# Optimization experiments

Measured on AMD Instinct MI355X. Metric: run time of the kernel, lower is better.

## Reference

```python
import jax, jax.numpy as jnp
import numpy as np

N = 50000
E = 640000
F_IN = 128
F_OUT = 128


def setup_inputs() -> dict:
    key = jax.random.key(0)
    k1, k2, k3, k4, k5 = jax.random.split(key, 5)
    x = jax.random.normal(k1, (N, F_IN), dtype=jnp.float32)
    edge_index = jax.random.randint(k2, (2, E), 0, N, dtype=jnp.int64)
    s = 1.0 / np.sqrt(F_IN)
    W_l = jax.random.uniform(k3, (F_IN, F_OUT), minval=-s, maxval=s, dtype=jnp.float32)
    W_r = jax.random.uniform(k4, (F_IN, F_OUT), minval=-s, maxval=s, dtype=jnp.float32)
    b = jax.random.uniform(k5, (F_OUT,), minval=-s, maxval=s, dtype=jnp.float32)
    return {"x": x, "edge_index": edge_index, "W_l": W_l, "W_r": W_r, "b": b}


def reference(x, edge_index, W_l, W_r, b):
    src, dst = edge_index[0], edge_index[1]
    # gather source-node features along edges: [E, F_in]
    msgs = x[src]
    # mean aggregation at destination nodes
    summed = jax.ops.segment_sum(msgs, dst, num_segments=N)          # [N, F_in]
    counts = jax.ops.segment_sum(jnp.ones((E,), jnp.float32), dst, num_segments=N)
    mean_nb = summed / jnp.maximum(counts, 1.0)[:, None]
    # SAGEConv: lin_l(aggregated) + lin_r(self), bias on lin_l only
    out = mean_nb @ W_l + x @ W_r + b
    return jax.nn.relu(out)
```

## Files before the change

kernel.cpp:

```cpp
#include <hip/hip_runtime.h>

#define N_NODES 50000
#define E_EDGES 640000
#define F 128

typedef __attribute__((ext_vector_type(8))) short short8;
typedef __attribute__((ext_vector_type(4))) float f32x4;

#define DEG_OFF 0
#define OFF_OFF 200704
#define CUR_OFF 401408
#define BSUM_OFF 601600
#define WF_OFF 603648
#define SRC_OFF 734720
#define XBF_OFF 3294720
#define MBF_OFF 16094720
#define WS_NEED_FULL 28894720ULL

#define XCAST_BLKS 3125
#define WPREP_BLKS 16
#define HIST_BLKS 2048
#define PREP_GRID (XCAST_BLKS + WPREP_BLKS + HIST_BLKS)

__device__ __forceinline__ unsigned short f2bf(float f) {
    unsigned int u = __builtin_bit_cast(unsigned int, f);
    u += 0x7FFFu + ((u >> 16) & 1u);
    return (unsigned short)(u >> 16);
}
__device__ __forceinline__ float bfhi2f(unsigned int hi16) {
    return __builtin_bit_cast(float, hi16 & 0xFFFF0000u);
}

__global__ __launch_bounds__(256) void gnn_prep(
    const float* __restrict__ x, const int* __restrict__ ei,
    const float* __restrict__ Wl, const float* __restrict__ Wr,
    short* __restrict__ Wf, unsigned short* __restrict__ xbf,
    int* __restrict__ deg, int full) {
    const int bid = blockIdx.x;
    const int t = threadIdx.x;
    if (bid < XCAST_BLKS) {
        if (!full) return;
        const size_t i = ((size_t)bid * 256 + t) * 8;
        const float4 a0 = *reinterpret_cast<const float4*>(x + i);
        const float4 a1 = *reinterpret_cast<const float4*>(x + i + 4);
        short8 v;
        v[0] = (short)f2bf(a0.x); v[1] = (short)f2bf(a0.y);
        v[2] = (short)f2bf(a0.z); v[3] = (short)f2bf(a0.w);
        v[4] = (short)f2bf(a1.x); v[5] = (short)f2bf(a1.y);
        v[6] = (short)f2bf(a1.z); v[7] = (short)f2bf(a1.w);
        *reinterpret_cast<short8*>((short*)xbf + i) = v;
    } else if (bid < XCAST_BLKS + WPREP_BLKS) {
        const int tid = (bid - XCAST_BLKS) * 256 + t;
        const int lane = tid & 63;
        const int frag = tid >> 6;
        const int kstep = frag >> 3;
        const int ct = frag & 7;
        const int kb = kstep * 32 + (lane >> 4) * 8;
        const int c = ct * 16 + (lane & 15);
        short8 v;
#pragma unroll
        for (int j = 0; j < 8; ++j) {
            const int k = kb + j;
            const float f = (k < F) ? Wl[k * F + c] : Wr[(k - F) * F + c];
            v[j] = (short)f2bf(f);
        }
        *reinterpret_cast<short8*>(Wf + (size_t)tid * 8) = v;
    } else {
        const int i = (bid - XCAST_BLKS - WPREP_BLKS) * 256 + t;
        const int stride = HIST_BLKS * 256;
        for (int e = i; e < E_EDGES; e += stride)
            atomicAdd(&deg[ei[E_EDGES + e]], 1);
    }
}

__global__ __launch_bounds__(256) void gnn_scan_a(const int* __restrict__ deg,
                                                  int* __restrict__ off,
                                                  int* __restrict__ bsum) {
    __shared__ int s[256];
    const int t = threadIdx.x;
    const int i = blockIdx.x * 256 + t;
    const int v = (i < N_NODES) ? deg[i] : 0;
    s[t] = v;
    __syncthreads();
    for (int d = 1; d < 256; d <<= 1) {
        const int u = (t >= d) ? s[t - d] : 0;
        __syncthreads();
        s[t] += u;
        __syncthreads();
    }
    if (i < N_NODES) off[i] = s[t] - v;
    if (t == 255) bsum[blockIdx.x] = s[255];
}

__global__ __launch_bounds__(256) void gnn_scan2(const int* __restrict__ bsum,
                                                 int* __restrict__ off,
                                                 int* __restrict__ cur) {
    __shared__ int s[256];
    const int t = threadIdx.x;
    const int bid = blockIdx.x;
    s[t] = (t < 196) ? bsum[t] : 0;
    __syncthreads();
    for (int d = 1; d < 256; d <<= 1) {
        const int u = (t >= d) ? s[t - d] : 0;
        __syncthreads();
        s[t] += u;
        __syncthreads();
    }
    const int myPre = (bid == 0) ? 0 : s[bid - 1];
    const int i = bid * 256 + t;
    if (i < N_NODES) {
        const int o = off[i] + myPre;
        off[i] = o;
        cur[i] = o;
    }
    if (bid == 0 && t == 0) off[N_NODES] = s[195];
}

__global__ __launch_bounds__(256) void gnn_fill(const int* __restrict__ ei,
                                                int* __restrict__ cur,
                                                int* __restrict__ srcs) {
    const int i = blockIdx.x * blockDim.x + threadIdx.x;
    const int stride = gridDim.x * blockDim.x;
    for (int e = i; e < E_EDGES; e += stride) {
        const int d = ei[E_EDGES + e];
        const int p = atomicAdd(&cur[d], 1);
        srcs[p] = ei[e];
    }
}

__global__ __launch_bounds__(256) void gnn_aggregate_bf(
    const unsigned short* __restrict__ xbf, const int* __restrict__ off,
    const int* __restrict__ srcs, unsigned short* __restrict__ mbf) {
    const int node = blockIdx.x * 4 + (threadIdx.x >> 6);
    if (node >= N_NODES) return;
    const int lane = threadIdx.x & 63;
    const int half = lane >> 5;
    const int l32 = lane & 31;
    const int o0 = off[node];
    const int o1 = off[node + 1];
    const unsigned short* xb = xbf + (size_t)l32 * 4;
    f32x4 acc0 = {0.f, 0.f, 0.f, 0.f}, acc1 = {0.f, 0.f, 0.f, 0.f};
    f32x4 acc2 = {0.f, 0.f, 0.f, 0.f}, acc3 = {0.f, 0.f, 0.f, 0.f};
    int j = o0;
    for (; j + 8 <= o1; j += 8) {
        const uint2 a = *reinterpret_cast<const uint2*>(xb + (size_t)srcs[j + half] * F);
        const uint2 b = *reinterpret_cast<const uint2*>(xb + (size_t)srcs[j + 2 + half] * F);
        const uint2 c = *reinterpret_cast<const uint2*>(xb + (size_t)srcs[j + 4 + half] * F);
        const uint2 d = *reinterpret_cast<const uint2*>(xb + (size_t)srcs[j + 6 + half] * F);
        acc0[0] += bfhi2f(a.x << 16); acc0[1] += bfhi2f(a.x);
        acc0[2] += bfhi2f(a.y << 16); acc0[3] += bfhi2f(a.y);
        acc1[0] += bfhi2f(b.x << 16); acc1[1] += bfhi2f(b.x);
        acc1[2] += bfhi2f(b.y << 16); acc1[3] += bfhi2f(b.y);
        acc2[0] += bfhi2f(c.x << 16); acc2[1] += bfhi2f(c.x);
        acc2[2] += bfhi2f(c.y << 16); acc2[3] += bfhi2f(c.y);
        acc3[0] += bfhi2f(d.x << 16); acc3[1] += bfhi2f(d.x);
        acc3[2] += bfhi2f(d.y << 16); acc3[3] += bfhi2f(d.y);
    }
    for (; j + 4 <= o1; j += 4) {
        const uint2 a = *reinterpret_cast<const uint2*>(xb + (size_t)srcs[j + half] * F);
        const uint2 b = *reinterpret_cast<const uint2*>(xb + (size_t)srcs[j + 2 + half] * F);
        acc0[0] += bfhi2f(a.x << 16); acc0[1] += bfhi2f(a.x);
        acc0[2] += bfhi2f(a.y << 16); acc0[3] += bfhi2f(a.y);
        acc1[0] += bfhi2f(b.x << 16); acc1[1] += bfhi2f(b.x);
        acc1[2] += bfhi2f(b.y << 16); acc1[3] += bfhi2f(b.y);
    }
    for (; j < o1; j += 2) {
        const int jj = j + half;
        const uint2 a = *reinterpret_cast<const uint2*>(
            xb + (size_t)srcs[(jj < o1) ? jj : o0] * F);
        if (jj < o1) {
            acc0[0] += bfhi2f(a.x << 16); acc0[1] += bfhi2f(a.x);
            acc0[2] += bfhi2f(a.y << 16); acc0[3] += bfhi2f(a.y);
        }
    }
    acc0 += acc1 + acc2 + acc3;
    f32x4 o;
    o[0] = __shfl_xor(acc0[0], 32, 64);
    o[1] = __shfl_xor(acc0[1], 32, 64);
    o[2] = __shfl_xor(acc0[2], 32, 64);
    o[3] = __shfl_xor(acc0[3], 32, 64);
    acc0 += o;
    if (half == 0) {
        const float inv = 1.0f / (float)max(o1 - o0, 1);
        acc0 *= inv;
        ushort4 m;
        m.x = f2bf(acc0[0]); m.y = f2bf(acc0[1]);
        m.z = f2bf(acc0[2]); m.w = f2bf(acc0[3]);
        *reinterpret_cast<ushort4*>(mbf + (size_t)node * F + l32 * 4) = m;
    }
}

__global__ __launch_bounds__(256) void gnn_finalize_bf(
    const unsigned short* __restrict__ xbf, const unsigned short* __restrict__ mbf,
    const short* __restrict__ Wf, const float* __restrict__ bias,
    float* __restrict__ out) {
    const int t = threadIdx.x;
    const int lane = t & 63;
    const int wv = t >> 6;
    const int r0 = blockIdx.x * 64 + wv * 16;
    const int rl = lane & 15;
    const int kg = lane >> 4;
    const int arow = r0 + rl;
    const int arow_c = (arow < N_NODES) ? arow : (N_NODES - 1);

    f32x4 acc[8];
#pragma unroll
    for (int ct = 0; ct < 8; ++ct) acc[ct] = (f32x4){0.f, 0.f, 0.f, 0.f};

#pragma unroll
    for (int kstep = 0; kstep < 8; ++kstep) {
        const int k0 = kstep * 32 + kg * 8;
        const unsigned short* asrc =
            (kstep < 4) ? (mbf + (size_t)arow_c * F + k0)
                        : (xbf + (size_t)arow_c * F + (k0 - F));
        const short8 af = *reinterpret_cast<const short8*>(asrc);
#pragma unroll
        for (int ct = 0; ct < 8; ++ct) {
            const short8 bf = *reinterpret_cast<const short8*>(
                Wf + (size_t)((kstep * 8 + ct) * 64 + lane) * 8);
            acc[ct] = __builtin_amdgcn_mfma_f32_16x16x32_bf16(af, bf, acc[ct],
                                                              0, 0, 0);
        }
    }

#pragma unroll
    for (int ct = 0; ct < 8; ++ct) {
        const int c = ct * 16 + rl;
        const float bv = bias[c];
#pragma unroll
        for (int r = 0; r < 4; ++r) {
            const int row = r0 + kg * 4 + r;
            if (row < N_NODES)
                out[(size_t)row * F + c] = fmaxf(acc[ct][r] + bv, 0.0f);
        }
    }
}

__global__ __launch_bounds__(256) void gnn_aggregate(
    const float* __restrict__ x, const int* __restrict__ off,
    const int* __restrict__ srcs, float* __restrict__ out) {
    const int node = blockIdx.x * 4 + (threadIdx.x >> 6);
    if (node >= N_NODES) return;
    const int lane = threadIdx.x & 63;
    const int half = lane >> 5;
    const int l32 = lane & 31;
    const int o0 = off[node];
    const int o1 = off[node + 1];
    f32x4 acc0 = {0.f, 0.f, 0.f, 0.f};
    f32x4 acc1 = {0.f, 0.f, 0.f, 0.f};
    int j = o0;
    for (; j + 4 <= o1; j += 4) {
        const int sA = srcs[j + half];
        const int sB = srcs[j + 2 + half];
        acc0 += *reinterpret_cast<const f32x4*>(x + (size_t)sA * F + l32 * 4);
        acc1 += *reinterpret_cast<const f32x4*>(x + (size_t)sB * F + l32 * 4);
    }
    for (; j < o1; j += 2) {
        const int jj = j + half;
        const int s = srcs[(jj < o1) ? jj : o0];
        f32x4 v = *reinterpret_cast<const f32x4*>(x + (size_t)s * F + l32 * 4);
        if (jj >= o1) v = (f32x4){0.f, 0.f, 0.f, 0.f};
        acc0 += v;
    }
    acc0 += acc1;
    f32x4 o;
    o[0] = __shfl_xor(acc0[0], 32, 64);
    o[1] = __shfl_xor(acc0[1], 32, 64);
    o[2] = __shfl_xor(acc0[2], 32, 64);
    o[3] = __shfl_xor(acc0[3], 32, 64);
    acc0 += o;
    if (half == 0) {
        const float inv = 1.0f / (float)max(o1 - o0, 1);
        acc0 *= inv;
        *reinterpret_cast<f32x4*>(out + (size_t)node * F + l32 * 4) = acc0;
    }
}

__global__ __launch_bounds__(256) void gnn_finalize_mfma(
    const float* __restrict__ x, const short* __restrict__ Wf,
    const float* __restrict__ bias, float* __restrict__ out) {
    const int t = threadIdx.x;
    const int lane = t & 63;
    const int wv = t >> 6;
    const int r0 = blockIdx.x * 64 + wv * 16;
    const int rl = lane & 15;
    const int kg = lane >> 4;
    const int arow = r0 + rl;
    const int arow_c = (arow < N_NODES) ? arow : (N_NODES - 1);
    f32x4 acc[8];
#pragma unroll
    for (int ct = 0; ct < 8; ++ct) acc[ct] = (f32x4){0.f, 0.f, 0.f, 0.f};
#pragma unroll
    for (int kstep = 0; kstep < 8; ++kstep) {
        const int k0 = kstep * 32 + kg * 8;
        const float* asrc = (kstep < 4) ? (out + (size_t)arow_c * F + k0)
                                        : (x + (size_t)arow_c * F + (k0 - F));
        const float4 a0 = *reinterpret_cast<const float4*>(asrc);
        const float4 a1 = *reinterpret_cast<const float4*>(asrc + 4);
        short8 af;
        af[0] = (short)f2bf(a0.x); af[1] = (short)f2bf(a0.y);
        af[2] = (short)f2bf(a0.z); af[3] = (short)f2bf(a0.w);
        af[4] = (short)f2bf(a1.x); af[5] = (short)f2bf(a1.y);
        af[6] = (short)f2bf(a1.z); af[7] = (short)f2bf(a1.w);
#pragma unroll
        for (int ct = 0; ct < 8; ++ct) {
            const short8 bf = *reinterpret_cast<const short8*>(
                Wf + (size_t)((kstep * 8 + ct) * 64 + lane) * 8);
            acc[ct] = __builtin_amdgcn_mfma_f32_16x16x32_bf16(af, bf, acc[ct],
                                                              0, 0, 0);
        }
    }
#pragma unroll
    for (int ct = 0; ct < 8; ++ct) {
        const int c = ct * 16 + rl;
        const float bv = bias[c];
#pragma unroll
        for (int r = 0; r < 4; ++r) {
            const int row = r0 + kg * 4 + r;
            if (row < N_NODES)
                out[(size_t)row * F + c] = fmaxf(acc[ct][r] + bv, 0.0f);
        }
    }
}

extern "C" void kernel_launch(void* const* d_in, const int* in_sizes, int n_in,
                              void* d_out, int out_size, void* d_ws,
                              size_t ws_size, hipStream_t stream) {
    const float* x = (const float*)d_in[0];
    const int* ei = (const int*)d_in[1];
    const float* Wl = (const float*)d_in[2];
    const float* Wr = (const float*)d_in[3];
    const float* b = (const float*)d_in[4];
    float* out = (float*)d_out;

    char* ws = (char*)d_ws;
    int* deg = (int*)(ws + DEG_OFF);
    int* off = (int*)(ws + OFF_OFF);
    int* cur = (int*)(ws + CUR_OFF);
    int* bsum = (int*)(ws + BSUM_OFF);
    short* Wf = (short*)(ws + WF_OFF);
    int* srcs = (int*)(ws + SRC_OFF);
    unsigned short* xbf = (unsigned short*)(ws + XBF_OFF);
    unsigned short* mbf = (unsigned short*)(ws + MBF_OFF);

    const int full = (ws_size >= WS_NEED_FULL) ? 1 : 0;

    hipMemsetAsync(deg, 0, N_NODES * sizeof(int), stream);
    gnn_prep<<<PREP_GRID, 256, 0, stream>>>(x, ei, Wl, Wr, Wf, xbf, deg, full);
    gnn_scan_a<<<196, 256, 0, stream>>>(deg, off, bsum);
    gnn_scan2<<<196, 256, 0, stream>>>(bsum, off, cur);
    gnn_fill<<<2048, 256, 0, stream>>>(ei, cur, srcs);

    if (full) {
        gnn_aggregate_bf<<<(N_NODES + 3) / 4, 256, 0, stream>>>(xbf, off, srcs,
                                                                mbf);
        gnn_finalize_bf<<<(N_NODES + 63) / 64, 256, 0, stream>>>(xbf, mbf, Wf,
                                                                 b, out);
    } else {
        gnn_aggregate<<<(N_NODES + 3) / 4, 256, 0, stream>>>(x, off, srcs, out);
        gnn_finalize_mfma<<<(N_NODES + 63) / 64, 256, 0, stream>>>(x, Wf, b,
                                                                   out);
    }
}
```

Measured before the change: 196.7 us.

## Move x/W casts into fill kernel and widen aggregate gathers to 16 bytes

Moves the x-to-bf16 cast and the weight repacking out of the histogram kernel and into the CSR fill kernel, with fill blocks placed first so the atomic scatter starts early. The histogram becomes its own small kernel. The aggregation kernel now has four 16-lane groups per wavefront each load 16-byte rows (uint4) instead of two halves loading 8 bytes, then reduces across groups with two shuffle stages. The intent is fewer, wider gather instructions and better overlap of the bandwidth-heavy cast with the atomic-bound fill, at the cost of an extra shuffle stage and more per-lane registers.

Result: slower. 201.0 us (+2.2%).

```diff
diff --git a/kernel.cpp b/kernel.cpp
--- a/kernel.cpp
+++ b/kernel.cpp
@@ -17,10 +17,10 @@
 #define MBF_OFF 16094720
 #define WS_NEED_FULL 28894720ULL
 
+#define FILL_BLKS 2048
+#define WPREP_BLKS 16
 #define XCAST_BLKS 3125
-#define WPREP_BLKS 16
-#define HIST_BLKS 2048
-#define PREP_GRID (XCAST_BLKS + WPREP_BLKS + HIST_BLKS)
+#define FXW_GRID (FILL_BLKS + WPREP_BLKS + XCAST_BLKS)
 
 __device__ __forceinline__ unsigned short f2bf(float f) {
     unsigned int u = __builtin_bit_cast(unsigned int, f);
@@ -31,46 +31,12 @@
     return __builtin_bit_cast(float, hi16 & 0xFFFF0000u);
 }
 
-__global__ __launch_bounds__(256) void gnn_prep(
-    const float* __restrict__ x, const int* __restrict__ ei,
-    const float* __restrict__ Wl, const float* __restrict__ Wr,
-    short* __restrict__ Wf, unsigned short* __restrict__ xbf,
-    int* __restrict__ deg, int full) {
-    const int bid = blockIdx.x;
-    const int t = threadIdx.x;
-    if (bid < XCAST_BLKS) {
-        if (!full) return;
-        const size_t i = ((size_t)bid * 256 + t) * 8;
-        const float4 a0 = *reinterpret_cast<const float4*>(x + i);
-        const float4 a1 = *reinterpret_cast<const float4*>(x + i + 4);
-        short8 v;
-        v[0] = (short)f2bf(a0.x); v[1] = (short)f2bf(a0.y);
-        v[2] = (short)f2bf(a0.z); v[3] = (short)f2bf(a0.w);
-        v[4] = (short)f2bf(a1.x); v[5] = (short)f2bf(a1.y);
-        v[6] = (short)f2bf(a1.z); v[7] = (short)f2bf(a1.w);
-        *reinterpret_cast<short8*>((short*)xbf + i) = v;
-    } else if (bid < XCAST_BLKS + WPREP_BLKS) {
-        const int tid = (bid - XCAST_BLKS) * 256 + t;
-        const int lane = tid & 63;
-        const int frag = tid >> 6;
-        const int kstep = frag >> 3;
-        const int ct = frag & 7;
-        const int kb = kstep * 32 + (lane >> 4) * 8;
-        const int c = ct * 16 + (lane & 15);
-        short8 v;
-#pragma unroll
-        for (int j = 0; j < 8; ++j) {
-            const int k = kb + j;
-            const float f = (k < F) ? Wl[k * F + c] : Wr[(k - F) * F + c];
-            v[j] = (short)f2bf(f);
-        }
-        *reinterpret_cast<short8*>(Wf + (size_t)tid * 8) = v;
-    } else {
-        const int i = (bid - XCAST_BLKS - WPREP_BLKS) * 256 + t;
-        const int stride = HIST_BLKS * 256;
-        for (int e = i; e < E_EDGES; e += stride)
-            atomicAdd(&deg[ei[E_EDGES + e]], 1);
-    }
+__global__ __launch_bounds__(256) void gnn_hist(const int* __restrict__ ei,
+                                                int* __restrict__ deg) {
+    const int i = blockIdx.x * blockDim.x + threadIdx.x;
+    const int stride = gridDim.x * blockDim.x;
+    for (int e = i; e < E_EDGES; e += stride)
+        atomicAdd(&deg[ei[E_EDGES + e]], 1);
 }
 
 __global__ __launch_bounds__(256) void gnn_scan_a(const int* __restrict__ deg,
@@ -116,17 +82,57 @@
     if (bid == 0 && t == 0) off[N_NODES] = s[195];
 }
 
-__global__ __launch_bounds__(256) void gnn_fill(const int* __restrict__ ei,
-                                                int* __restrict__ cur,
-                                                int* __restrict__ srcs) {
-    const int i = blockIdx.x * blockDim.x + threadIdx.x;
-    const int stride = gridDim.x * blockDim.x;
-    for (int e = i; e < E_EDGES; e += stride) {
-        const int d = ei[E_EDGES + e];
-        const int p = atomicAdd(&cur[d], 1);
-        srcs[p] = ei[e];
-    }
-}
+__global__ __launch_bounds__(256) void gnn_fill_xw(
+    const int* __restrict__ ei, int* __restrict__ cur, int* __restrict__ srcs,
+    const float* __restrict__ x, const float* __restrict__ Wl,
+    const float* __restrict__ Wr, short* __restrict__ Wf,
+    unsigned short* __restrict__ xbf, int full) {
+    const int bid = blockIdx.x;
+    const int t = threadIdx.x;
+    if (bid < FILL_BLKS) {
+        const int i = bid * 256 + t;
+        const int stride = FILL_BLKS * 256;
+        for (int e = i; e < E_EDGES; e += stride) {
+            const int d = ei[E_EDGES + e];
+            const int p = atomicAdd(&cur[d], 1);
+            srcs[p] = ei[e];
+        }
+    } else if (bid < FILL_BLKS + WPREP_BLKS) {
+        const int tid = (bid - FILL_BLKS) * 256 + t;
+        const int lane = tid & 63;
+        const int frag = tid >> 6;
+        const int kstep = frag >> 3;
+        const int ct = frag & 7;
+        const int kb = kstep * 32 + (lane >> 4) * 8;
+        const int c = ct * 16 + (lane & 15);
+        short8 v;
+#pragma unroll
+        for (int j = 0; j < 8; ++j) {
+            const int k = kb + j;
+            const float f = (k < F) ? Wl[k * F + c] : Wr[(k - F) * F + c];
+            v[j] = (short)f2bf(f);
+        }
+        *reinterpret_cast<short8*>(Wf + (size_t)tid * 8) = v;
+    } else {
+        if (!full) return;
+        const size_t i =
+            ((size_t)(bid - FILL_BLKS - WPREP_BLKS) * 256 + t) * 8;
+        const float4 a0 = *reinterpret_cast<const float4*>(x + i);
+        const float4 a1 = *reinterpret_cast<const float4*>(x + i + 4);
+        short8 v;
+        v[0] = (short)f2bf(a0.x); v[1] = (short)f2bf(a0.y);
+        v[2] = (short)f2bf(a0.z); v[3] = (short)f2bf(a0.w);
+        v[4] = (short)f2bf(a1.x); v[5] = (short)f2bf(a1.y);
+        v[6] = (short)f2bf(a1.z); v[7] = (short)f2bf(a1.w);
+        *reinterpret_cast<short8*>((short*)xbf + i) = v;
+    }
+}
+
+#define ACCQ(u, A0, A1)                                        \
+    A0[0] += bfhi2f(u.x << 16); A0[1] += bfhi2f(u.x);          \
+    A0[2] += bfhi2f(u.y << 16); A0[3] += bfhi2f(u.y);          \
+    A1[0] += bfhi2f(u.z << 16); A1[1] += bfhi2f(u.z);          \
+    A1[2] += bfhi2f(u.w << 16); A1[3] += bfhi2f(u.w);
 
 __global__ __launch_bounds__(256) void gnn_aggregate_bf(
     const unsigned short* __restrict__ xbf, const int* __restrict__ off,
@@ -134,59 +140,58 @@
     const int node = blockIdx.x * 4 + (threadIdx.x >> 6);
     if (node >= N_NODES) return;
     const int lane = threadIdx.x & 63;
-    const int half = lane >> 5;
-    const int l32 = lane & 31;
+    const int grp = lane >> 4;
+    const int l16 = lane & 15;
     const int o0 = off[node];
     const int o1 = off[node + 1];
-    const unsigned short* xb = xbf + (size_t)l32 * 4;
-    f32x4 acc0 = {0.f, 0.f, 0.f, 0.f}, acc1 = {0.f, 0.f, 0.f, 0.f};
-    f32x4 acc2 = {0.f, 0.f, 0.f, 0.f}, acc3 = {0.f, 0.f, 0.f, 0.f};
+    const unsigned short* xb = xbf + l16 * 8;
+    f32x4 a0 = {0.f, 0.f, 0.f, 0.f}, a1 = {0.f, 0.f, 0.f, 0.f};
+    f32x4 b0 = {0.f, 0.f, 0.f, 0.f}, b1 = {0.f, 0.f, 0.f, 0.f};
     int j = o0;
     for (; j + 8 <= o1; j += 8) {
-        const uint2 a = *reinterpret_cast<const uint2*>(xb + (size_t)srcs[j + half] * F);
-        const uint2 b = *reinterpret_cast<const uint2*>(xb + (size_t)srcs[j + 2 + half] * F);
-        const uint2 c = *reinterpret_cast<const uint2*>(xb + (size_t)srcs[j + 4 + half] * F);
-        const uint2 d = *reinterpret_cast<const uint2*>(xb + (size_t)srcs[j + 6 + half] * F);
-        acc0[0] += bfhi2f(a.x << 16); acc0[1] += bfhi2f(a.x);
-        acc0[2] += bfhi2f(a.y << 16); acc0[3] += bfhi2f(a.y);
-        acc1[0] += bfhi2f(b.x << 16); acc1[1] += bfhi2f(b.x);
-        acc1[2] += bfhi2f(b.y << 16); acc1[3] += bfhi2f(b.y);
-        acc2[0] += bfhi2f(c.x << 16); acc2[1] += bfhi2f(c.x);
-        acc2[2] += bfhi2f(c.y << 16); acc2[3] += bfhi2f(c.y);
-        acc3[0] += bfhi2f(d.x << 16); acc3[1] += bfhi2f(d.x);
-        acc3[2] += bfhi2f(d.y << 16); acc3[3] += bfhi2f(d.y);
-    }
-    for (; j + 4 <= o1; j += 4) {
-        const uint2 a = *reinterpret_cast<const uint2*>(xb + (size_t)srcs[j + half] * F);
-        const uint2 b = *reinterpret_cast<const uint2*>(xb + (size_t)srcs[j + 2 + half] * F);
-        acc0[0] += bfhi2f(a.x << 16); acc0[1] += bfhi2f(a.x);
-        acc0[2] += bfhi2f(a.y << 16); acc0[3] += bfhi2f(a.y);
-        acc1[0] += bfhi2f(b.x << 16); acc1[1] += bfhi2f(b.x);
-        acc1[2] += bfhi2f(b.y << 16); acc1[3] += bfhi2f(b.y);
-    }
-    for (; j < o1; j += 2) {
-        const int jj = j + half;
-        const uint2 a = *reinterpret_cast<const uint2*>(
+        const uint4 u =
+            *reinterpret_cast<const uint4*>(xb + (size_t)srcs[j + grp] * F);
+        const uint4 v =
+            *reinterpret_cast<const uint4*>(xb + (size_t)srcs[j + 4 + grp] * F);
+        ACCQ(u, a0, a1);
+        ACCQ(v, b0, b1);
+    }
+    if (j + 4 <= o1) {
+        const uint4 u =
+            *reinterpret_cast<const uint4*>(xb + (size_t)srcs[j + grp] * F);
+        ACCQ(u, a0, a1);
+        j += 4;
+    }
+    if (j < o1) {
+        const int jj = j + grp;
+        const uint4 u = *reinterpret_cast<const uint4*>(
             xb + (size_t)srcs[(jj < o1) ? jj : o0] * F);
-        if (jj < o1) {
-            acc0[0] += bfhi2f(a.x << 16); acc0[1] += bfhi2f(a.x);
-            acc0[2] += bfhi2f(a.y << 16); acc0[3] += bfhi2f(a.y);
-        }
-    }
-    acc0 += acc1 + acc2 + acc3;
-    f32x4 o;
-    o[0] = __shfl_xor(acc0[0], 32, 64);
-    o[1] = __shfl_xor(acc0[1], 32, 64);
-    o[2] = __shfl_xor(acc0[2], 32, 64);
-    o[3] = __shfl_xor(acc0[3], 32, 64);
-    acc0 += o;
-    if (half == 0) {
+        if (jj < o1) { ACCQ(u, b0, b1); }
+    }
+    a0 += b0;
+    a1 += b1;
+    f32x4 t0, t1;
+#pragma unroll
+    for (int i = 0; i < 4; ++i) {
+        t0[i] = __shfl_xor(a0[i], 16, 64);
+        t1[i] = __shfl_xor(a1[i], 16, 64);
+    }
+    a0 += t0; a1 += t1;
+#pragma unroll
+    for (int i = 0; i < 4; ++i) {
+        t0[i] = __shfl_xor(a0[i], 32, 64);
+        t1[i] = __shfl_xor(a1[i], 32, 64);
+    }
+    a0 += t0; a1 += t1;
+    if (grp == 0) {
         const float inv = 1.0f / (float)max(o1 - o0, 1);
-        acc0 *= inv;
-        ushort4 m;
-        m.x = f2bf(acc0[0]); m.y = f2bf(acc0[1]);
-        m.z = f2bf(acc0[2]); m.w = f2bf(acc0[3]);
-        *reinterpret_cast<ushort4*>(mbf + (size_t)node * F + l32 * 4) = m;
+        a0 *= inv; a1 *= inv;
+        uint4 m;
+        m.x = (unsigned)f2bf(a0[0]) | ((unsigned)f2bf(a0[1]) << 16);
+        m.y = (unsigned)f2bf(a0[2]) | ((unsigned)f2bf(a0[3]) << 16);
+        m.z = (unsigned)f2bf(a1[0]) | ((unsigned)f2bf(a1[1]) << 16);
+        m.w = (unsigned)f2bf(a1[2]) | ((unsigned)f2bf(a1[3]) << 16);
+        *reinterpret_cast<uint4*>(mbf + (size_t)node * F + l16 * 8) = m;
     }
 }
 
@@ -346,10 +351,11 @@
     const int full = (ws_size >= WS_NEED_FULL) ? 1 : 0;
 
     hipMemsetAsync(deg, 0, N_NODES * sizeof(int), stream);
-    gnn_prep<<<PREP_GRID, 256, 0, stream>>>(x, ei, Wl, Wr, Wf, xbf, deg, full);
+    gnn_hist<<<2048, 256, 0, stream>>>(ei, deg);
     gnn_scan_a<<<196, 256, 0, stream>>>(deg, off, bsum);
     gnn_scan2<<<196, 256, 0, stream>>>(bsum, off, cur);
-    gnn_fill<<<2048, 256, 0, stream>>>(ei, cur, srcs);
+    gnn_fill_xw<<<FXW_GRID, 256, 0, stream>>>(ei, cur, srcs, x, Wl, Wr, Wf,
+                                              xbf, full);
 
     if (full) {
         gnn_aggregate_bf<<<(N_NODES + 3) / 4, 256, 0, stream>>>(xbf, off, srcs,
```
